# Optimization experiments

Hardware: AMD Instinct MI355X
Metric: run time of the kernel (lower is better)

Reference implementation:

```python
import jax, jax.numpy as jnp
import numpy as np

B, S, D, H = 4, 2048, 1024, 16
DH = D // H  # depth per head


def setup_inputs() -> dict:
    key = jax.random.key(0)
    ks = jax.random.split(key, 12)
    s = 1.0 / np.sqrt(D)
    return {
        "v": jax.random.normal(ks[0], (B, S, D), jnp.float32),
        "k": jax.random.normal(ks[1], (B, S, D), jnp.float32),
        "q": jax.random.normal(ks[2], (B, S, D), jnp.float32),
        "mask": jnp.ones((B, 1, S, S), jnp.float32),
        "wq_w": jax.random.normal(ks[3], (D, D), jnp.float32) * s,
        "wq_b": jnp.zeros((D,), jnp.float32),
        "wk_w": jax.random.normal(ks[4], (D, D), jnp.float32) * s,
        "wk_b": jnp.zeros((D,), jnp.float32),
        "wv_w": jax.random.normal(ks[5], (D, D), jnp.float32) * s,
        "wv_b": jnp.zeros((D,), jnp.float32),
        "wo_w": jax.random.normal(ks[6], (D, D), jnp.float32) * s,
        "wo_b": jnp.zeros((D,), jnp.float32),
    }


def _split_heads(x):
    # [B, S, D] -> [B, H, S, DH]
    b, s, _ = x.shape
    return x.reshape(b, s, H, DH).transpose(0, 2, 1, 3)


def reference(v, k, q, mask, wq_w, wq_b, wk_w, wk_b, wv_w, wv_b, wo_w, wo_b):
    qh = _split_heads(q @ wq_w + wq_b)
    kh = _split_heads(k @ wk_w + wk_b)
    vh = _split_heads(v @ wv_w + wv_b)
    # scaled dot-product attention with multiplicative custom mask
    logits = jnp.einsum("bhqd,bhkd->bhqk", qh, kh) / jnp.sqrt(jnp.float32(DH))
    logits = logits * mask - 1e6 * (1.0 - mask)
    attn_weights = jax.nn.softmax(logits, axis=-1)
    ctx = jnp.einsum("bhqk,bhkd->bhqd", attn_weights, vh)
    concat = ctx.transpose(0, 2, 1, 3).reshape(-1, q.shape[1], D)
    out = concat @ wo_w + wo_b
    return out, attn_weights
```

## Files before the change

kernel.cpp:

```cpp
#include <hip/hip_runtime.h>


typedef unsigned short u16;
typedef unsigned int   u32;
typedef u16   u16x4  __attribute__((ext_vector_type(4)));
typedef u16   u16x8  __attribute__((ext_vector_type(8)));
typedef int   i32x4  __attribute__((ext_vector_type(4)));
typedef float f32x4  __attribute__((ext_vector_type(4)));
typedef __bf16 bf16x8 __attribute__((ext_vector_type(8)));

#define GLDS16(gp, lp)                                                         \
  __builtin_amdgcn_global_load_lds(                                            \
      (const __attribute__((address_space(1))) void*)(gp),                     \
      (__attribute__((address_space(3))) void*)(lp), 16, 0, 0)

__device__ __forceinline__ u16 f2bf(float x) {
  __bf16 h = (__bf16)x;
  union { __bf16 h; u16 u; } c; c.h = h; return c.u;
}
__device__ __forceinline__ void nt_store4(float* p, f32x4 v) {
  __builtin_nontemporal_store(v, (f32x4*)p);
}

static const int Bn = 4, Sn = 2048, Dn = 1024, Hn = 16, DHn = 64;
#define MASK_NEG (-1442695.0f)

__global__ __launch_bounds__(256) void prep_k(
    const float* __restrict__ q, const float* __restrict__ k,
    const float* __restrict__ v, const float* __restrict__ mask,
    const float* __restrict__ w0, const float* __restrict__ w1,
    const float* __restrict__ w2, const float* __restrict__ w3,
    u16* __restrict__ qkv, u16* __restrict__ WTb, int* __restrict__ flags) {
  __shared__ __align__(16) u16 tile[64][72];
  __shared__ int ok_s;
  int bid = blockIdx.x, t = threadIdx.x;

  if (bid < 12288) {
    int which = bid >> 12;
    size_t li = (size_t)(bid & 4095) * 256 + t;
    const float* src = which == 0 ? q : which == 1 ? k : v;
    const f32x4* p = (const f32x4*)src + li * 2;
    f32x4 a = p[0], b = p[1];
    u16x8 r;
    r[0]=f2bf(a[0]); r[1]=f2bf(a[1]); r[2]=f2bf(a[2]); r[3]=f2bf(a[3]);
    r[4]=f2bf(b[0]); r[5]=f2bf(b[1]); r[6]=f2bf(b[2]); r[7]=f2bf(b[3]);
    *((u16x8*)(qkv + (size_t)which * 8388608) + li) = r;
  } else if (bid < 13312) {
    int i = bid - 12288;
    int z = i >> 8, rem = i & 255, bx = rem & 15, by = rem >> 4;
    const float* W = z == 0 ? w0 : z == 1 ? w1 : z == 2 ? w2 : w3;
    u16* WT = WTb + (size_t)z * 1048576;
    for (int rr = 0; rr < 4; rr++) {
      int r = rr * 16 + (t >> 4);
      int c = (t & 15) * 4;
      float4 vv = *(const float4*)(W + (size_t)(by * 64 + r) * 1024 + bx * 64 + c);
      tile[c + 0][r] = f2bf(vv.x); tile[c + 1][r] = f2bf(vv.y);
      tile[c + 2][r] = f2bf(vv.z); tile[c + 3][r] = f2bf(vv.w);
    }
    __syncthreads();
    for (int rr = 0; rr < 2; rr++) {
      int gid = rr * 256 + t;
      int r = gid >> 3, g = gid & 7;
      u16x8 vv = *(const u16x8*)&tile[r][g * 8];
      *(u16x8*)(WT + (size_t)(bx * 64 + r) * 1024 + by * 64 + g * 8) = vv;
    }
  } else {
    int i = bid - 13312;
    int qt = i & 15, kt = (i >> 4) & 31, b = i >> 9;
    if (t == 0) ok_s = 1;
    __syncthreads();
    const float* base = mask + ((size_t)b * Sn + qt * 128) * Sn + kt * 64;
    int r = t >> 1, c0 = (t & 1) * 32;
    const float* p = base + (size_t)r * Sn + c0;
    bool ok = true;
    for (int j = 0; j < 8; j++) {
      float4 vv = *(const float4*)(p + j * 4);
      ok = ok && (vv.x == 1.0f) && (vv.y == 1.0f) && (vv.z == 1.0f) && (vv.w == 1.0f);
    }
    if (!ok) atomicAnd(&ok_s, 0);
    __syncthreads();
    if (t == 0) flags[(b * 32 + kt) * 16 + qt] = ok_s;
  }
}

__device__ __forceinline__ void gemm_body(const u16* __restrict__ A,
                                          const u16* __restrict__ BT,
                                          const float* __restrict__ bias,
                                          void* __restrict__ outp, int mode,
                                          int nt, int mt, char* sm) {
  const int K = 1024;
  int m0 = mt * 128, n0 = nt * 128;
  int tid = threadIdx.x, w = tid >> 6, l = tid & 63, l15 = l & 15, l4 = l >> 4;
  int wm = w >> 1, wn = w & 1;

  size_t goff_a[4], goff_b[4];
  int lbase[4];
  for (int i = 0; i < 4; i++) {
    int gi = (w * 4 + i) * 64 + l;
    int row = gi >> 3, g = gi & 7;
    int gx = g ^ (row & 7);
    goff_a[i] = (size_t)(m0 + row) * K + gx * 8;
    goff_b[i] = (size_t)(n0 + row) * K + gx * 8;
    lbase[i] = (w * 4 + i) * 1024;
  }

  f32x4 acc[4][4] = {};
  for (int t = 0; t < 16; t++) {
    int k0 = t * 64;
    for (int i = 0; i < 4; i++) {
      GLDS16(A + goff_a[i] + k0, sm + lbase[i]);
      GLDS16(BT + goff_b[i] + k0, sm + 16384 + lbase[i]);
    }
    __syncthreads();
#pragma unroll
    for (int kk = 0; kk < 2; kk++) {
      int kb = kk * 64 + l4 * 16;
      bf16x8 af[4], bf[4];
#pragma unroll
      for (int mi = 0; mi < 4; mi++) {
        int row = wm * 64 + mi * 16 + l15;
        af[mi] = *(const bf16x8*)(sm + row * 128 + (kb ^ ((row & 7) << 4)));
      }
#pragma unroll
      for (int nj = 0; nj < 4; nj++) {
        int row = wn * 64 + nj * 16 + l15;
        bf[nj] = *(const bf16x8*)(sm + 16384 + row * 128 + (kb ^ ((row & 7) << 4)));
      }
#pragma unroll
      for (int mi = 0; mi < 4; mi++)
#pragma unroll
        for (int nj = 0; nj < 4; nj++)
          acc[mi][nj] = __builtin_amdgcn_mfma_f32_16x16x32_bf16(af[mi], bf[nj], acc[mi][nj], 0, 0, 0);
    }
    __syncthreads();
  }

  if (mode == 3) {
    float* out = (float*)outp;
#pragma unroll
    for (int mi = 0; mi < 4; mi++)
#pragma unroll
      for (int nj = 0; nj < 4; nj++)
#pragma unroll
        for (int r = 0; r < 4; r++) {
          int mg = m0 + wm * 64 + mi * 16 + l4 * 4 + r;
          int ng = n0 + wn * 64 + nj * 16 + l15;
          __builtin_nontemporal_store(acc[mi][nj][r] + bias[ng],
                                      out + (size_t)mg * 1024 + ng);
        }
  } else if (mode == 2) {
    u16* vt = (u16*)outp;
#pragma unroll
    for (int mi = 0; mi < 4; mi++)
#pragma unroll
      for (int nj = 0; nj < 4; nj++) {
        int ng = n0 + wn * 64 + nj * 16 + l15;
        int h = ng >> 6, d = ng & 63;
        int mgb = m0 + wm * 64 + mi * 16 + l4 * 4;
        int b = mgb >> 11, s = mgb & 2047;
        float bs = bias[ng];
        u16x4 pk;
#pragma unroll
        for (int r = 0; r < 4; r++) pk[r] = f2bf(acc[mi][nj][r] + bs);
        *(u16x4*)(vt + ((size_t)(b * Hn + h) * DHn + d) * Sn + s) = pk;
      }
  } else {
    u16* oh = (u16*)outp;
    float sc = (mode == 0) ? 0.18033688f : 1.0f;
#pragma unroll
    for (int mi = 0; mi < 4; mi++)
#pragma unroll
      for (int nj = 0; nj < 4; nj++) {
        int ng = n0 + wn * 64 + nj * 16 + l15;
        int h = ng >> 6, d = ng & 63;
        float bs = bias[ng];
#pragma unroll
        for (int r = 0; r < 4; r++) {
          int mg = m0 + wm * 64 + mi * 16 + l4 * 4 + r;
          int b = mg >> 11, s = mg & 2047;
          oh[((size_t)(b * Hn + h) * Sn + s) * DHn + d] = f2bf((acc[mi][nj][r] + bs) * sc);
        }
      }
  }
}

__global__ __launch_bounds__(256) void gemmO_k(const u16* __restrict__ A,
                                               const u16* __restrict__ BT,
                                               const float* __restrict__ bias,
                                               float* __restrict__ outp) {
  __shared__ __align__(16) char sm[32768];
  int hw = blockIdx.x;
  int lg = (hw & 7) * 64 + (hw >> 3);
  int nt = lg & 7, mt = lg >> 3;
  gemm_body(A, BT, bias, (void*)outp, 3, nt, mt, sm);
}

__global__ __launch_bounds__(256) void gemm3_k(const u16* __restrict__ Ab,
                                               const u16* __restrict__ BTb,
                                               const float* __restrict__ b0,
                                               const float* __restrict__ b1,
                                               const float* __restrict__ b2,
                                               u16* __restrict__ outb) {
  __shared__ __align__(16) char sm[32768];
  int hw = blockIdx.x;
  int lg = (hw & 7) * 192 + (hw >> 3);
  int z = lg >> 9, r = lg & 511;
  int nt = r & 7, mt = r >> 3;
  const u16* A = Ab + (size_t)z * 8388608;
  const u16* BT = BTb + (size_t)z * 1048576;
  const float* bias = z == 0 ? b0 : z == 1 ? b1 : b2;
  u16* out = outb + (size_t)z * 8388608;
  gemm_body(A, BT, bias, (void*)out, z, nt, mt, sm);
}

#define K0_OFF 0
#define K1_OFF 8192
#define V0_OFF 16384
#define V1_OFF 24576
#define P_OFF  32768

__global__ __launch_bounds__(256) void attn_k(
    const u16* __restrict__ qh, const u16* __restrict__ kh,
    const u16* __restrict__ vt, const float* __restrict__ mask,
    const int* __restrict__ flags, float* __restrict__ attn,
    u16* __restrict__ ctxc) {
  __shared__ __align__(16) char sm[49152];
  int hw = blockIdx.x;
  int lg = (hw & 7) * 128 + (hw >> 3);
  int qt = lg & 15, h = (lg >> 4) & 15, b = lg >> 8;
  int bh = b * Hn + h;
  int tid = threadIdx.x, w = tid >> 6, l = tid & 63, l15 = l & 15, l4 = l >> 4;

  const u16* Qg = qh + ((size_t)bh * Sn + qt * 128) * DHn;
  const u16* Kg = kh + (size_t)bh * Sn * DHn;
  const u16* Vg = vt + (size_t)bh * DHn * Sn;
  const float* Mg = mask + (size_t)b * Sn * Sn + (size_t)(qt * 128) * Sn;

  u32 fl = (u32)__ballot(l < 32 && flags[(b * 32 + l) * 16 + qt] != 0);

  int srowA[4], sgxA[4], sdstA[4];
  for (int i = 0; i < 4; i++) {
    int gid = i * 256 + tid, row = gid >> 3, g = gid & 7;
    srowA[i] = row; sgxA[i] = (g ^ (row & 7)) * 8; sdstA[i] = gid * 16;
  }
#define STAGE_KA(t, buf)                                                       \
  for (int i = 0; i < 4; i++)                                                  \
    GLDS16(Kg + (size_t)((t) * 128 + srowA[i]) * DHn + sgxA[i], sm + (buf) + sdstA[i]);
#define STAGE_K(t, buf)                                                        \
  for (int i = 0; i < 2; i++)                                                  \
    GLDS16(Kg + (size_t)((t) * 64 + srowA[i]) * DHn + sgxA[i], sm + (buf) + sdstA[i]);
#define STAGE_V(t, buf)                                                        \
  for (int i = 0; i < 2; i++)                                                  \
    GLDS16(Vg + (size_t)srowA[i] * Sn + (t) * 64 + sgxA[i], sm + (buf) + sdstA[i]);

  bf16x8 qf[2][2];
#pragma unroll
  for (int ni = 0; ni < 2; ni++)
#pragma unroll
    for (int kk = 0; kk < 2; kk++)
      qf[ni][kk] = *(const bf16x8*)(Qg + (size_t)(w * 32 + ni * 16 + l15) * DHn + kk * 32 + l4 * 8);

  float lsum[2] = {0.f, 0.f};
  STAGE_KA(0, 0);
  for (int t = 0; t < 16; t++) {
    int kcur = (t & 1) ? 16384 : 0;
    __syncthreads();
    if (t < 15) { int knxt = (t & 1) ? 0 : 16384; STAGE_KA(t + 1, knxt); }
#pragma unroll
    for (int h2 = 0; h2 < 2; h2++) {
      int kt = t * 2 + h2;
      f32x4 s[4][2] = {};
#pragma unroll
      for (int kk = 0; kk < 2; kk++) {
        int kb = kk * 64 + l4 * 16;
        bf16x8 a[4];
#pragma unroll
        for (int mi = 0; mi < 4; mi++) {
          int row = h2 * 64 + mi * 16 + l15;
          a[mi] = *(const bf16x8*)(sm + kcur + row * 128 + (kb ^ ((row & 7) << 4)));
        }
#pragma unroll
        for (int mi = 0; mi < 4; mi++)
#pragma unroll
          for (int ni = 0; ni < 2; ni++)
            s[mi][ni] = __builtin_amdgcn_mfma_f32_16x16x32_bf16(a[mi], qf[ni][kk], s[mi][ni], 0, 0, 0);
      }
      if (!((fl >> kt) & 1)) {
#pragma unroll
        for (int ni = 0; ni < 2; ni++) {
          const float* mrow = Mg + (size_t)(w * 32 + ni * 16 + l15) * Sn + kt * 64;
#pragma unroll
          for (int mi = 0; mi < 4; mi++) {
            f32x4 mv = *(const f32x4*)(mrow + mi * 16 + l4 * 4);
#pragma unroll
            for (int r = 0; r < 4; r++)
              s[mi][ni][r] = s[mi][ni][r] * mv[r] + MASK_NEG * (1.f - mv[r]);
          }
        }
      }
#pragma unroll
      for (int ni = 0; ni < 2; ni++)
#pragma unroll
        for (int mi = 0; mi < 4; mi++)
#pragma unroll
          for (int r = 0; r < 4; r++) lsum[ni] += __builtin_exp2f(s[mi][ni][r]);
    }
  }
  float cv[2];
#pragma unroll
  for (int ni = 0; ni < 2; ni++) {
    lsum[ni] += __shfl_xor(lsum[ni], 16);
    lsum[ni] += __shfl_xor(lsum[ni], 32);
    cv[ni] = __builtin_log2f(lsum[ni]);
  }

  __syncthreads();
  f32x4 ctx[4][2] = {};
  STAGE_K(0, K0_OFF);
  STAGE_V(0, V0_OFF);
  for (int t = 0; t < 32; t++) {
    int kcur = (t & 1) ? K1_OFF : K0_OFF;
    int vcur = (t & 1) ? V1_OFF : V0_OFF;
    __syncthreads();
    if (t < 31) {
      int knxt = (t & 1) ? K0_OFF : K1_OFF;
      int vnxt = (t & 1) ? V0_OFF : V1_OFF;
      STAGE_K(t + 1, knxt);
      STAGE_V(t + 1, vnxt);
    }
    f32x4 s[4][2] = {};
#pragma unroll
    for (int kk = 0; kk < 2; kk++) {
      int kb = kk * 64 + l4 * 16;
      bf16x8 a[4];
#pragma unroll
      for (int mi = 0; mi < 4; mi++) {
        int row = mi * 16 + l15;
        a[mi] = *(const bf16x8*)(sm + kcur + row * 128 + (kb ^ ((row & 7) << 4)));
      }
#pragma unroll
      for (int mi = 0; mi < 4; mi++)
#pragma unroll
        for (int ni = 0; ni < 2; ni++)
          s[mi][ni] = __builtin_amdgcn_mfma_f32_16x16x32_bf16(a[mi], qf[ni][kk], s[mi][ni], 0, 0, 0);
    }
    if (!((fl >> t) & 1)) {
#pragma unroll
      for (int ni = 0; ni < 2; ni++) {
        const float* mrow = Mg + (size_t)(w * 32 + ni * 16 + l15) * Sn + t * 64;
#pragma unroll
        for (int mi = 0; mi < 4; mi++) {
          f32x4 mv = *(const f32x4*)(mrow + mi * 16 + l4 * 4);
#pragma unroll
          for (int r = 0; r < 4; r++)
            s[mi][ni][r] = s[mi][ni][r] * mv[r] + MASK_NEG * (1.f - mv[r]);
        }
      }
    }
#pragma unroll
    for (int ni = 0; ni < 2; ni++)
#pragma unroll
      for (int mi = 0; mi < 4; mi++)
#pragma unroll
        for (int r = 0; r < 4; r++) s[mi][ni][r] = __builtin_exp2f(s[mi][ni][r] - cv[ni]);
#pragma unroll
    for (int ni = 0; ni < 2; ni++) {
      float* arow = attn + ((size_t)bh * Sn + qt * 128 + w * 32 + ni * 16 + l15) * Sn + t * 64;
#pragma unroll
      for (int mi = 0; mi < 4; mi++)
        nt_store4(arow + mi * 16 + l4 * 4, s[mi][ni]);
    }
#pragma unroll
    for (int ni = 0; ni < 2; ni++) {
      int q = w * 32 + ni * 16 + l15;
#pragma unroll
      for (int mi = 0; mi < 4; mi++) {
        u16x4 pk;
#pragma unroll
        for (int r = 0; r < 4; r++) pk[r] = f2bf(s[mi][ni][r]);
        int kb = mi * 32 + l4 * 8;
        *(u16x4*)(sm + P_OFF + q * 128 + (kb ^ ((q & 7) << 4))) = pk;
      }
    }
#pragma unroll
    for (int kk = 0; kk < 2; kk++) {
      int kb = kk * 64 + l4 * 16;
      bf16x8 av[4], bp[2];
#pragma unroll
      for (int mi = 0; mi < 4; mi++) {
        int row = mi * 16 + l15;
        av[mi] = *(const bf16x8*)(sm + vcur + row * 128 + (kb ^ ((row & 7) << 4)));
      }
#pragma unroll
      for (int ni = 0; ni < 2; ni++) {
        int q = w * 32 + ni * 16 + l15;
        bp[ni] = *(const bf16x8*)(sm + P_OFF + q * 128 + (kb ^ ((q & 7) << 4)));
      }
#pragma unroll
      for (int mi = 0; mi < 4; mi++)
#pragma unroll
        for (int ni = 0; ni < 2; ni++)
          ctx[mi][ni] = __builtin_amdgcn_mfma_f32_16x16x32_bf16(av[mi], bp[ni], ctx[mi][ni], 0, 0, 0);
    }
  }

#pragma unroll
  for (int ni = 0; ni < 2; ni++) {
    int q = w * 32 + ni * 16 + l15;
#pragma unroll
    for (int mi = 0; mi < 4; mi++) {
      u16x4 ck;
#pragma unroll
      for (int r = 0; r < 4; r++) ck[r] = f2bf(ctx[mi][ni][r]);
      int db = mi * 32 + l4 * 8;
      *(u16x4*)(sm + P_OFF + q * 128 + (db ^ ((q & 7) << 4))) = ck;
    }
  }
  __syncthreads();
  {
    int q = tid >> 1, hf = tid & 1;
    u16* dst = ctxc + ((size_t)b * Sn + qt * 128 + q) * Dn + h * DHn + hf * 32;
#pragma unroll
    for (int c4 = 0; c4 < 4; c4++) {
      int db = hf * 64 + c4 * 16;
      i32x4 v = *(const i32x4*)(sm + P_OFF + q * 128 + (db ^ ((q & 7) << 4)));
      *(i32x4*)(dst + c4 * 8) = v;
    }
  }
}

extern "C" void kernel_launch(void* const* d_in, const int* in_sizes, int n_in,
                              void* d_out, int out_size, void* d_ws, size_t ws_size,
                              hipStream_t stream) {
  const float* v_f  = (const float*)d_in[0];
  const float* k_f  = (const float*)d_in[1];
  const float* q_f  = (const float*)d_in[2];
  const float* mask = (const float*)d_in[3];
  const float* wq_w = (const float*)d_in[4];
  const float* wq_b = (const float*)d_in[5];
  const float* wk_w = (const float*)d_in[6];
  const float* wk_b = (const float*)d_in[7];
  const float* wv_w = (const float*)d_in[8];
  const float* wv_b = (const float*)d_in[9];
  const float* wo_w = (const float*)d_in[10];
  const float* wo_b = (const float*)d_in[11];

  char* ws = (char*)d_ws;
  u16*   qbf  = (u16*)(ws + 0);
  u16*   wT   = (u16*)(ws + 50331648);
  u16*   woT  = (u16*)(ws + 56623104);
  u16*   qhp  = (u16*)(ws + 58720256);
  u16*   khp  = (u16*)(ws + 75497472);
  u16*   vtp  = (u16*)(ws + 92274688);
  u16*   ctxc = (u16*)(ws + 109051904);
  int*   flg  = (int*)(ws + 125829120);

  float* out  = (float*)d_out;
  float* attn = out + (size_t)Bn * Sn * Dn;

  prep_k<<<15360, 256, 0, stream>>>(q_f, k_f, v_f, mask,
                                    wq_w, wk_w, wv_w, wo_w, qbf, wT, flg);
  gemm3_k<<<1536, 256, 0, stream>>>(qbf, wT, wq_b, wk_b, wv_b, qhp);
  attn_k<<<1024, 256, 0, stream>>>(qhp, khp, vtp, mask, flg, attn, ctxc);
  gemmO_k<<<512, 256, 0, stream>>>(ctxc, woT, wo_b, out);
}
```

Measured before the change: 564.9 us.

## Shrink P scratch to per-wave slot and use vmcnt-based tile barrier

The attention loop now gives each wave a private 16-row P slot, reused for both ni halves, instead of a 128-row shared P buffer. This cuts LDS from 48KB to 40KB, which may allow more resident blocks. V operands are preloaded into registers before the P writes, and the per-iteration __syncthreads is replaced by a custom barrier that waits only until vmcnt(8), leaving later global loads in flight. The epilogue reuses the K buffer region for the ctx transpose. The partial vmcnt wait relies on an exact count of outstanding memory ops, including the nontemporal attn stores, so a wrong count could read stale LDS.

```diff
diff --git a/kernel.cpp b/kernel.cpp
--- a/kernel.cpp
+++ b/kernel.cpp
@@ -219,12 +219,22 @@
 #define V1_OFF 24576
 #define P_OFF  32768
 
+#define TILE_SYNC()                                                            \
+  do {                                                                         \
+    __builtin_amdgcn_sched_barrier(0);                                         \
+    asm volatile("s_waitcnt vmcnt(8)" ::: "memory");                           \
+    __builtin_amdgcn_sched_barrier(0);                                         \
+    __builtin_amdgcn_s_barrier();                                              \
+    asm volatile("" ::: "memory");                                             \
+    __builtin_amdgcn_sched_barrier(0);                                         \
+  } while (0)
+
 __global__ __launch_bounds__(256) void attn_k(
     const u16* __restrict__ qh, const u16* __restrict__ kh,
     const u16* __restrict__ vt, const float* __restrict__ mask,
     const int* __restrict__ flags, float* __restrict__ attn,
     u16* __restrict__ ctxc) {
-  __shared__ __align__(16) char sm[49152];
+  __shared__ __align__(16) char sm[40960];
   int hw = blockIdx.x;
   int lg = (hw & 7) * 128 + (hw >> 3);
   int qt = lg & 15, h = (lg >> 4) & 15, b = lg >> 8;
@@ -318,10 +328,10 @@
   f32x4 ctx[4][2] = {};
   STAGE_K(0, K0_OFF);
   STAGE_V(0, V0_OFF);
+  __syncthreads();
   for (int t = 0; t < 32; t++) {
     int kcur = (t & 1) ? K1_OFF : K0_OFF;
     int vcur = (t & 1) ? V1_OFF : V0_OFF;
-    __syncthreads();
     if (t < 31) {
       int knxt = (t & 1) ? K0_OFF : K1_OFF;
       int vnxt = (t & 1) ? V0_OFF : V1_OFF;
@@ -370,60 +380,59 @@
       for (int mi = 0; mi < 4; mi++)
         nt_store4(arow + mi * 16 + l4 * 4, s[mi][ni]);
     }
+    bf16x8 av[4][2];
+#pragma unroll
+    for (int kk = 0; kk < 2; kk++) {
+      int kb = kk * 64 + l4 * 16;
+#pragma unroll
+      for (int mi = 0; mi < 4; mi++) {
+        int row = mi * 16 + l15;
+        av[mi][kk] = *(const bf16x8*)(sm + vcur + row * 128 + (kb ^ ((row & 7) << 4)));
+      }
+    }
+    int slot = w * 16 + l15;
 #pragma unroll
     for (int ni = 0; ni < 2; ni++) {
-      int q = w * 32 + ni * 16 + l15;
 #pragma unroll
       for (int mi = 0; mi < 4; mi++) {
         u16x4 pk;
 #pragma unroll
         for (int r = 0; r < 4; r++) pk[r] = f2bf(s[mi][ni][r]);
         int kb = mi * 32 + l4 * 8;
-        *(u16x4*)(sm + P_OFF + q * 128 + (kb ^ ((q & 7) << 4))) = pk;
-      }
-    }
-#pragma unroll
-    for (int kk = 0; kk < 2; kk++) {
-      int kb = kk * 64 + l4 * 16;
-      bf16x8 av[4], bp[2];
-#pragma unroll
-      for (int mi = 0; mi < 4; mi++) {
-        int row = mi * 16 + l15;
-        av[mi] = *(const bf16x8*)(sm + vcur + row * 128 + (kb ^ ((row & 7) << 4)));
-      }
-#pragma unroll
-      for (int ni = 0; ni < 2; ni++) {
-        int q = w * 32 + ni * 16 + l15;
-        bp[ni] = *(const bf16x8*)(sm + P_OFF + q * 128 + (kb ^ ((q & 7) << 4)));
-      }
-#pragma unroll
-      for (int mi = 0; mi < 4; mi++)
-#pragma unroll
-        for (int ni = 0; ni < 2; ni++)
-          ctx[mi][ni] = __builtin_amdgcn_mfma_f32_16x16x32_bf16(av[mi], bp[ni], ctx[mi][ni], 0, 0, 0);
-    }
+        *(u16x4*)(sm + P_OFF + slot * 128 + (kb ^ ((slot & 7) << 4))) = pk;
+      }
+#pragma unroll
+      for (int kk = 0; kk < 2; kk++) {
+        int kb = kk * 64 + l4 * 16;
+        bf16x8 bp = *(const bf16x8*)(sm + P_OFF + slot * 128 + (kb ^ ((slot & 7) << 4)));
+#pragma unroll
+        for (int mi = 0; mi < 4; mi++)
+          ctx[mi][ni] = __builtin_amdgcn_mfma_f32_16x16x32_bf16(av[mi][kk], bp, ctx[mi][ni], 0, 0, 0);
+      }
+    }
+    TILE_SYNC();
   }
 
 #pragma unroll
   for (int ni = 0; ni < 2; ni++) {
-    int q = w * 32 + ni * 16 + l15;
+    int qrow = w * 32 + ni * 16 + l15;
 #pragma unroll
     for (int mi = 0; mi < 4; mi++) {
       u16x4 ck;
 #pragma unroll
       for (int r = 0; r < 4; r++) ck[r] = f2bf(ctx[mi][ni][r]);
       int db = mi * 32 + l4 * 8;
-      *(u16x4*)(sm + P_OFF + q * 128 + (db ^ ((q & 7) << 4))) = ck;
+      *(u16x4*)(sm + qrow * 128 + (db ^ ((qrow & 7) << 4))) = ck;
     }
   }
   __syncthreads();
   {
-    int q = tid >> 1, hf = tid & 1;
-    u16* dst = ctxc + ((size_t)b * Sn + qt * 128 + q) * Dn + h * DHn + hf * 32;
+    int qrow = tid >> 1, hf = tid & 1;
+    u16* dst = ctxc + ((size_t)b * Sn + qt * 128 + qrow) * Dn + h * DHn + hf * 32;
 #pragma unroll
     for (int c4 = 0; c4 < 4; c4++) {
       int db = hf * 64 + c4 * 16;
-      i32x4 v = *(const i32x4*)(sm + P_OFF + q * 128 + (db ^ ((q & 7) << 4)));
+      i32x4 v = *(const i32x4*)(sm + qrow * 128 + (db ^ ((qrow & 7) << 4)));
       *(i32x4*)(dst + c4 * 8) = v;
     }
   }
```

Result: slower. 576.7 us (+2.1%).

## Process two query tiles per attention block, overlapping second tile's row-sum pass

Applied to the files above, without the earlier changes.

Each attention block now covers two 128-row query tiles instead of one, and the grid shrinks from 1024 to 512 blocks. The row-sum pass for the second tile is fused into the output pass of the first tile, so K is streamed three times per pair of tiles instead of four. The ctx write-out is moved into a shared helper, and the kernel declares a minimum of two blocks per SM in its launch bounds. The aim is less K traffic and fewer launches; the cost is more registers per thread (two Q fragment sets and two score sets) and fewer blocks to hide latency, while the large attention-weight stores stay unchanged.

```diff
diff --git a/kernel.cpp b/kernel.cpp
--- a/kernel.cpp
+++ b/kernel.cpp
@@ -219,24 +219,56 @@
 #define V1_OFF 24576
 #define P_OFF  32768
 
-__global__ __launch_bounds__(256) void attn_k(
+__device__ __forceinline__ void ctx_epilogue(f32x4 (*ctx)[2], char* sm,
+                                             u16* ctxc, int b, int h, int qtv,
+                                             int w, int l15, int l4, int tid) {
+#pragma unroll
+  for (int ni = 0; ni < 2; ni++) {
+    int q = w * 32 + ni * 16 + l15;
+#pragma unroll
+    for (int mi = 0; mi < 4; mi++) {
+      u16x4 ck;
+#pragma unroll
+      for (int r = 0; r < 4; r++) ck[r] = f2bf(ctx[mi][ni][r]);
+      int db = mi * 32 + l4 * 8;
+      *(u16x4*)(sm + P_OFF + q * 128 + (db ^ ((q & 7) << 4))) = ck;
+    }
+  }
+  __syncthreads();
+  {
+    int q = tid >> 1, hf = tid & 1;
+    u16* dst = ctxc + ((size_t)b * Sn + qtv * 128 + q) * Dn + h * DHn + hf * 32;
+#pragma unroll
+    for (int c4 = 0; c4 < 4; c4++) {
+      int db = hf * 64 + c4 * 16;
+      i32x4 v = *(const i32x4*)(sm + P_OFF + q * 128 + (db ^ ((q & 7) << 4)));
+      *(i32x4*)(dst + c4 * 8) = v;
+    }
+  }
+}
+
+__global__ __launch_bounds__(256, 2) void attn_k(
     const u16* __restrict__ qh, const u16* __restrict__ kh,
     const u16* __restrict__ vt, const float* __restrict__ mask,
     const int* __restrict__ flags, float* __restrict__ attn,
     u16* __restrict__ ctxc) {
   __shared__ __align__(16) char sm[49152];
   int hw = blockIdx.x;
-  int lg = (hw & 7) * 128 + (hw >> 3);
-  int qt = lg & 15, h = (lg >> 4) & 15, b = lg >> 8;
+  int lg = (hw & 7) * 64 + (hw >> 3);
+  int qp = lg & 7, h = (lg >> 3) & 15, b = lg >> 7;
+  int qt0 = qp * 2, qt1 = qp * 2 + 1;
   int bh = b * Hn + h;
   int tid = threadIdx.x, w = tid >> 6, l = tid & 63, l15 = l & 15, l4 = l >> 4;
 
-  const u16* Qg = qh + ((size_t)bh * Sn + qt * 128) * DHn;
   const u16* Kg = kh + (size_t)bh * Sn * DHn;
   const u16* Vg = vt + (size_t)bh * DHn * Sn;
-  const float* Mg = mask + (size_t)b * Sn * Sn + (size_t)(qt * 128) * Sn;
-
-  u32 fl = (u32)__ballot(l < 32 && flags[(b * 32 + l) * 16 + qt] != 0);
+  const u16* Qg0 = qh + ((size_t)bh * Sn + qt0 * 128) * DHn;
+  const u16* Qg1 = qh + ((size_t)bh * Sn + qt1 * 128) * DHn;
+  const float* Mg0 = mask + (size_t)b * Sn * Sn + (size_t)(qt0 * 128) * Sn;
+  const float* Mg1 = mask + (size_t)b * Sn * Sn + (size_t)(qt1 * 128) * Sn;
+
+  u32 fl0 = (u32)__ballot(l < 32 && flags[(b * 32 + l) * 16 + qt0] != 0);
+  u32 fl1 = (u32)__ballot(l < 32 && flags[(b * 32 + l) * 16 + qt1] != 0);
 
   int srowA[4], sgxA[4], sdstA[4];
   for (int i = 0; i < 4; i++) {
@@ -253,14 +285,16 @@
   for (int i = 0; i < 2; i++)                                                  \
     GLDS16(Vg + (size_t)srowA[i] * Sn + (t) * 64 + sgxA[i], sm + (buf) + sdstA[i]);
 
-  bf16x8 qf[2][2];
+  bf16x8 qf0[2][2], qf1[2][2];
 #pragma unroll
   for (int ni = 0; ni < 2; ni++)
 #pragma unroll
-    for (int kk = 0; kk < 2; kk++)
-      qf[ni][kk] = *(const bf16x8*)(Qg + (size_t)(w * 32 + ni * 16 + l15) * DHn + kk * 32 + l4 * 8);
-
-  float lsum[2] = {0.f, 0.f};
+    for (int kk = 0; kk < 2; kk++) {
+      qf0[ni][kk] = *(const bf16x8*)(Qg0 + (size_t)(w * 32 + ni * 16 + l15) * DHn + kk * 32 + l4 * 8);
+      qf1[ni][kk] = *(const bf16x8*)(Qg1 + (size_t)(w * 32 + ni * 16 + l15) * DHn + kk * 32 + l4 * 8);
+    }
+
+  float lsum0[2] = {0.f, 0.f};
   STAGE_KA(0, 0);
   for (int t = 0; t < 16; t++) {
     int kcur = (t & 1) ? 16384 : 0;
@@ -283,12 +317,12 @@
         for (int mi = 0; mi < 4; mi++)
 #pragma unroll
           for (int ni = 0; ni < 2; ni++)
-            s[mi][ni] = __builtin_amdgcn_mfma_f32_16x16x32_bf16(a[mi], qf[ni][kk], s[mi][ni], 0, 0, 0);
-      }
-      if (!((fl >> kt) & 1)) {
+            s[mi][ni] = __builtin_amdgcn_mfma_f32_16x16x32_bf16(a[mi], qf0[ni][kk], s[mi][ni], 0, 0, 0);
+      }
+      if (!((fl0 >> kt) & 1)) {
 #pragma unroll
         for (int ni = 0; ni < 2; ni++) {
-          const float* mrow = Mg + (size_t)(w * 32 + ni * 16 + l15) * Sn + kt * 64;
+          const float* mrow = Mg0 + (size_t)(w * 32 + ni * 16 + l15) * Sn + kt * 64;
 #pragma unroll
           for (int mi = 0; mi < 4; mi++) {
             f32x4 mv = *(const f32x4*)(mrow + mi * 16 + l4 * 4);
@@ -303,19 +337,20 @@
 #pragma unroll
         for (int mi = 0; mi < 4; mi++)
 #pragma unroll
-          for (int r = 0; r < 4; r++) lsum[ni] += __builtin_exp2f(s[mi][ni][r]);
-    }
-  }
-  float cv[2];
+          for (int r = 0; r < 4; r++) lsum0[ni] += __builtin_exp2f(s[mi][ni][r]);
+    }
+  }
+  float cv0[2];
 #pragma unroll
   for (int ni = 0; ni < 2; ni++) {
-    lsum[ni] += __shfl_xor(lsum[ni], 16);
-    lsum[ni] += __shfl_xor(lsum[ni], 32);
-    cv[ni] = __builtin_log2f(lsum[ni]);
+    lsum0[ni] += __shfl_xor(lsum0[ni], 16);
+    lsum0[ni] += __shfl_xor(lsum0[ni], 32);
+    cv0[ni] = __builtin_log2f(lsum0[ni]);
   }
 
   __syncthreads();
   f32x4 ctx[4][2] = {};
+  float lsum1[2] = {0.f, 0.f};
   STAGE_K(0, K0_OFF);
   STAGE_V(0, V0_OFF);
   for (int t = 0; t < 32; t++) {
@@ -328,7 +363,7 @@
       STAGE_K(t + 1, knxt);
       STAGE_V(t + 1, vnxt);
     }
-    f32x4 s[4][2] = {};
+    f32x4 s0[4][2] = {}, s1[4][2] = {};
 #pragma unroll
     for (int kk = 0; kk < 2; kk++) {
       int kb = kk * 64 + l4 * 16;
@@ -341,18 +376,140 @@
 #pragma unroll
       for (int mi = 0; mi < 4; mi++)
 #pragma unroll
-        for (int ni = 0; ni < 2; ni++)
-          s[mi][ni] = __builtin_amdgcn_mfma_f32_16x16x32_bf16(a[mi], qf[ni][kk], s[mi][ni], 0, 0, 0);
-    }
-    if (!((fl >> t) & 1)) {
+        for (int ni = 0; ni < 2; ni++) {
+          s0[mi][ni] = __builtin_amdgcn_mfma_f32_16x16x32_bf16(a[mi], qf0[ni][kk], s0[mi][ni], 0, 0, 0);
+          s1[mi][ni] = __builtin_amdgcn_mfma_f32_16x16x32_bf16(a[mi], qf1[ni][kk], s1[mi][ni], 0, 0, 0);
+        }
+    }
+    if (!((fl0 >> t) & 1)) {
 #pragma unroll
       for (int ni = 0; ni < 2; ni++) {
-        const float* mrow = Mg + (size_t)(w * 32 + ni * 16 + l15) * Sn + t * 64;
+        const float* mrow = Mg0 + (size_t)(w * 32 + ni * 16 + l15) * Sn + t * 64;
 #pragma unroll
         for (int mi = 0; mi < 4; mi++) {
           f32x4 mv = *(const f32x4*)(mrow + mi * 16 + l4 * 4);
 #pragma unroll
           for (int r = 0; r < 4; r++)
+            s0[mi][ni][r] = s0[mi][ni][r] * mv[r] + MASK_NEG * (1.f - mv[r]);
+        }
+      }
+    }
+    if (!((fl1 >> t) & 1)) {
+#pragma unroll
+      for (int ni = 0; ni < 2; ni++) {
+        const float* mrow = Mg1 + (size_t)(w * 32 + ni * 16 + l15) * Sn + t * 64;
+#pragma unroll
+        for (int mi = 0; mi < 4; mi++) {
+          f32x4 mv = *(const f32x4*)(mrow + mi * 16 + l4 * 4);
+#pragma unroll
+          for (int r = 0; r < 4; r++)
+            s1[mi][ni][r] = s1[mi][ni][r] * mv[r] + MASK_NEG * (1.f - mv[r]);
+        }
+      }
+    }
+#pragma unroll
+    for (int ni = 0; ni < 2; ni++)
+#pragma unroll
+      for (int mi = 0; mi < 4; mi++)
+#pragma unroll
+        for (int r = 0; r < 4; r++) s0[mi][ni][r] = __builtin_exp2f(s0[mi][ni][r] - cv0[ni]);
+#pragma unroll
+    for (int ni = 0; ni < 2; ni++) {
+      float* arow = attn + ((size_t)bh * Sn + qt0 * 128 + w * 32 + ni * 16 + l15) * Sn + t * 64;
+#pragma unroll
+      for (int mi = 0; mi < 4; mi++)
+        nt_store4(arow + mi * 16 + l4 * 4, s0[mi][ni]);
+    }
+#pragma unroll
+    for (int ni = 0; ni < 2; ni++) {
+      int q = w * 32 + ni * 16 + l15;
+#pragma unroll
+      for (int mi = 0; mi < 4; mi++) {
+        u16x4 pk;
+#pragma unroll
+        for (int r = 0; r < 4; r++) pk[r] = f2bf(s0[mi][ni][r]);
+        int kb = mi * 32 + l4 * 8;
+        *(u16x4*)(sm + P_OFF + q * 128 + (kb ^ ((q & 7) << 4))) = pk;
+      }
+    }
+#pragma unroll
+    for (int ni = 0; ni < 2; ni++)
+#pragma unroll
+      for (int mi = 0; mi < 4; mi++)
+#pragma unroll
+        for (int r = 0; r < 4; r++) lsum1[ni] += __builtin_exp2f(s1[mi][ni][r]);
+#pragma unroll
+    for (int kk = 0; kk < 2; kk++) {
+      int kb = kk * 64 + l4 * 16;
+      bf16x8 av[4], bp[2];
+#pragma unroll
+      for (int mi = 0; mi < 4; mi++) {
+        int row = mi * 16 + l15;
+        av[mi] = *(const bf16x8*)(sm + vcur + row * 128 + (kb ^ ((row & 7) << 4)));
+      }
+#pragma unroll
+      for (int ni = 0; ni < 2; ni++) {
+        int q = w * 32 + ni * 16 + l15;
+        bp[ni] = *(const bf16x8*)(sm + P_OFF + q * 128 + (kb ^ ((q & 7) << 4)));
+      }
+#pragma unroll
+      for (int mi = 0; mi < 4; mi++)
+#pragma unroll
+        for (int ni = 0; ni < 2; ni++)
+          ctx[mi][ni] = __builtin_amdgcn_mfma_f32_16x16x32_bf16(av[mi], bp[ni], ctx[mi][ni], 0, 0, 0);
+    }
+  }
+  float cv1[2];
+#pragma unroll
+  for (int ni = 0; ni < 2; ni++) {
+    lsum1[ni] += __shfl_xor(lsum1[ni], 16);
+    lsum1[ni] += __shfl_xor(lsum1[ni], 32);
+    cv1[ni] = __builtin_log2f(lsum1[ni]);
+  }
+
+  STAGE_K(0, K0_OFF);
+  STAGE_V(0, V0_OFF);
+  ctx_epilogue(ctx, sm, ctxc, b, h, qt0, w, l15, l4, tid);
+
+#pragma unroll
+  for (int mi = 0; mi < 4; mi++)
+#pragma unroll
+    for (int ni = 0; ni < 2; ni++) ctx[mi][ni] = (f32x4){0.f, 0.f, 0.f, 0.f};
+  for (int t = 0; t < 32; t++) {
+    int kcur = (t & 1) ? K1_OFF : K0_OFF;
+    int vcur = (t & 1) ? V1_OFF : V0_OFF;
+    __syncthreads();
+    if (t < 31) {
+      int knxt = (t & 1) ? K0_OFF : K1_OFF;
+      int vnxt = (t & 1) ? V0_OFF : V1_OFF;
+      STAGE_K(t + 1, knxt);
+      STAGE_V(t + 1, vnxt);
+    }
+    f32x4 s[4][2] = {};
+#pragma unroll
+    for (int kk = 0; kk < 2; kk++) {
+      int kb = kk * 64 + l4 * 16;
+      bf16x8 a[4];
+#pragma unroll
+      for (int mi = 0; mi < 4; mi++) {
+        int row = mi * 16 + l15;
+        a[mi] = *(const bf16x8*)(sm + kcur + row * 128 + (kb ^ ((row & 7) << 4)));
+      }
+#pragma unroll
+      for (int mi = 0; mi < 4; mi++)
+#pragma unroll
+        for (int ni = 0; ni < 2; ni++)
+          s[mi][ni] = __builtin_amdgcn_mfma_f32_16x16x32_bf16(a[mi], qf1[ni][kk], s[mi][ni], 0, 0, 0);
+    }
+    if (!((fl1 >> t) & 1)) {
+#pragma unroll
+      for (int ni = 0; ni < 2; ni++) {
+        const float* mrow = Mg1 + (size_t)(w * 32 + ni * 16 + l15) * Sn + t * 64;
+#pragma unroll
+        for (int mi = 0; mi < 4; mi++) {
+          f32x4 mv = *(const f32x4*)(mrow + mi * 16 + l4 * 4);
+#pragma unroll
+          for (int r = 0; r < 4; r++)
             s[mi][ni][r] = s[mi][ni][r] * mv[r] + MASK_NEG * (1.f - mv[r]);
         }
       }
@@ -362,10 +519,10 @@
 #pragma unroll
       for (int mi = 0; mi < 4; mi++)
 #pragma unroll
-        for (int r = 0; r < 4; r++) s[mi][ni][r] = __builtin_exp2f(s[mi][ni][r] - cv[ni]);
+        for (int r = 0; r < 4; r++) s[mi][ni][r] = __builtin_exp2f(s[mi][ni][r] - cv1[ni]);
 #pragma unroll
     for (int ni = 0; ni < 2; ni++) {
-      float* arow = attn + ((size_t)bh * Sn + qt * 128 + w * 32 + ni * 16 + l15) * Sn + t * 64;
+      float* arow = attn + ((size_t)bh * Sn + qt1 * 128 + w * 32 + ni * 16 + l15) * Sn + t * 64;
 #pragma unroll
       for (int mi = 0; mi < 4; mi++)
         nt_store4(arow + mi * 16 + l4 * 4, s[mi][ni]);
@@ -403,30 +560,8 @@
           ctx[mi][ni] = __builtin_amdgcn_mfma_f32_16x16x32_bf16(av[mi], bp[ni], ctx[mi][ni], 0, 0, 0);
     }
   }
-
-#pragma unroll
-  for (int ni = 0; ni < 2; ni++) {
-    int q = w * 32 + ni * 16 + l15;
-#pragma unroll
-    for (int mi = 0; mi < 4; mi++) {
-      u16x4 ck;
-#pragma unroll
-      for (int r = 0; r < 4; r++) ck[r] = f2bf(ctx[mi][ni][r]);
-      int db = mi * 32 + l4 * 8;
-      *(u16x4*)(sm + P_OFF + q * 128 + (db ^ ((q & 7) << 4))) = ck;
-    }
-  }
   __syncthreads();
-  {
-    int q = tid >> 1, hf = tid & 1;
-    u16* dst = ctxc + ((size_t)b * Sn + qt * 128 + q) * Dn + h * DHn + hf * 32;
-#pragma unroll
-    for (int c4 = 0; c4 < 4; c4++) {
-      int db = hf * 64 + c4 * 16;
-      i32x4 v = *(const i32x4*)(sm + P_OFF + q * 128 + (db ^ ((q & 7) << 4)));
-      *(i32x4*)(dst + c4 * 8) = v;
-    }
-  }
+  ctx_epilogue(ctx, sm, ctxc, b, h, qt1, w, l15, l4, tid);
 }
 
 extern "C" void kernel_launch(void* const* d_in, const int* in_sizes, int n_in,
@@ -461,6 +596,6 @@
   prep_k<<<15360, 256, 0, stream>>>(q_f, k_f, v_f, mask,
                                     wq_w, wk_w, wv_w, wo_w, qbf, wT, flg);
   gemm3_k<<<1536, 256, 0, stream>>>(qbf, wT, wq_b, wk_b, wv_b, qhp);
-  attn_k<<<1024, 256, 0, stream>>>(qhp, khp, vtp, mask, flg, attn, ctxc);
+  attn_k<<<512, 256, 0, stream>>>(qhp, khp, vtp, mask, flg, attn, ctxc);
   gemmO_k<<<512, 256, 0, stream>>>(ctxc, woT, wo_b, out);
 }
```

Result: slower. 647.7 us (+14.7%).
